# Kernel optimization log

Measured on AMD Instinct MI355X. Metric: run time of the kernel, lower is better.

## Reference

```python
import jax, jax.numpy as jnp
import numpy as np
from jax import lax

B, TS, NN, FC = 16, 16, 4096, 1
HIDDEN = 64


def setup_inputs() -> dict:
    key = jax.random.key(0)
    k1, k2, k3, k4, k5 = jax.random.split(key, 5)
    x = jax.random.normal(k1, (B, TS, NN, FC), dtype=jnp.float32)
    # Conv2d(in_ch + hidden -> 4*hidden, kernel=3, padding=1), OIHW layout
    conv_w = jax.random.normal(k2, (4 * HIDDEN, FC + HIDDEN, 3, 3), dtype=jnp.float32) * 0.05
    conv_b = jax.random.normal(k3, (4 * HIDDEN,), dtype=jnp.float32) * 0.05
    # fc: Conv2d(hidden -> 1, kernel=1)
    fc_w = jax.random.normal(k4, (1, HIDDEN, 1, 1), dtype=jnp.float32) * 0.05
    fc_b = jax.random.normal(k5, (1,), dtype=jnp.float32) * 0.05
    return {"x": x, "conv_w": conv_w, "conv_b": conv_b, "fc_w": fc_w, "fc_b": fc_b}


def _convlstm_forward(x, conv_w, conv_b, fc_w, fc_b):
    Bb, Ts, Nn, Fc = x.shape
    hidden = fc_w.shape[1]
    # [B, Ts, Fc, Nn, 1] -> scan over time axis: [Ts, B, Fc, Nn, 1]
    xp = jnp.transpose(x, (0, 1, 3, 2))[..., None]
    xs = jnp.swapaxes(xp, 0, 1)
    h0 = jnp.zeros((Bb, hidden, Nn, 1), dtype=x.dtype)
    c0 = jnp.zeros_like(h0)

    dn = lax.conv_dimension_numbers(h0.shape[:1] + (Fc + hidden, Nn, 1), conv_w.shape, ("NCHW", "OIHW", "NCHW"))

    def step(carry, xt):
        h, c = carry
        inp = jnp.concatenate([xt, h], axis=1)  # [B, Fc+hidden, Nn, 1]
        gates = lax.conv_general_dilated(inp, conv_w, (1, 1), ((1, 1), (1, 1)), dimension_numbers=dn)
        gates = gates + conv_b[None, :, None, None]
        i, f, o, g = jnp.split(gates, 4, axis=1)
        c2 = jax.nn.sigmoid(f) * c + jax.nn.sigmoid(i) * jnp.tanh(g)
        h2 = jax.nn.sigmoid(o) * jnp.tanh(c2)
        return (h2, c2), None

    (h, c), _ = lax.scan(step, (h0, c0), xs)
    # fc: 1x1 conv -> [B, 1, Nn, 1]
    out = jnp.einsum("bchw,oc->bohw", h, fc_w[:, :, 0, 0]) + fc_b[None, :, None, None]
    out = out[..., 0]                 # [B, 1, Nn]
    out = jnp.transpose(out, (0, 2, 1))[:, None]  # [B, 1, Nn, 1]
    return jnp.broadcast_to(out, (Bb, Ts, Nn, 1))


def reference(x, conv_w, conv_b, fc_w, fc_b):
    return _convlstm_forward(x, conv_w, conv_b, fc_w, fc_b)
```

## Files before the change

kernel.cpp:

```cpp
#include <hip/hip_runtime.h>

typedef _Float16 f16;
typedef __attribute__((ext_vector_type(8))) _Float16 half8;
typedef __attribute__((ext_vector_type(4))) float floatx4;

#define BB    16
#define TSN   16
#define NNP   4096
#define HID   64
#define KPK   224
#define WOUT  128
#define HALO  16
#define WCMP  160
#define HROWS 162
#define NMS   10
#define NTIL  32

#define LOG2E 1.44269504088896340736f

__device__ __forceinline__ int hadr(int rr, int c) {
    return rr * 64 + ((c ^ (rr & 7)) << 3);
}
__device__ __forceinline__ unsigned f16pair(float a, float b) {
    union { f16 h; unsigned short u; } ua, ub;
    ua.h = (f16)a; ub.h = (f16)b;
    return (unsigned)ua.u | ((unsigned)ub.u << 16);
}
__device__ __forceinline__ unsigned pkrtz(float a, float b) {
    typedef __fp16 h2v __attribute__((ext_vector_type(2)));
    h2v r = __builtin_amdgcn_cvt_pkrtz(a, b);
    union { h2v h; unsigned u; } cv; cv.h = r; return cv.u;
}

__device__ __forceinline__ float fast_exp2(float x) {
#if __has_builtin(__builtin_amdgcn_exp2f)
    return __builtin_amdgcn_exp2f(x);
#else
    return exp2f(x);
#endif
}
__device__ __forceinline__ float fast_rcp(float x) {
#if __has_builtin(__builtin_amdgcn_rcpf)
    return __builtin_amdgcn_rcpf(x);
#else
    return 1.0f / x;
#endif
}

__device__ __forceinline__ float dpp_xor8(float v) {
    return __int_as_float(__builtin_amdgcn_mov_dpp(__float_as_int(v), 0x128, 0xF, 0xF, true));
}
__device__ __forceinline__ float dpp_xor1(float v) {
    return __int_as_float(__builtin_amdgcn_mov_dpp(__float_as_int(v), 0xB1, 0xF, 0xF, true));
}

__global__ void pack_w_kernel(const float* __restrict__ conv_w,
                              const float* __restrict__ conv_b,
                              f16* __restrict__ wpack) {
    int idx = blockIdx.x * 256 + threadIdx.x;
    if (idx >= 4 * 64 * KPK) return;
    int k  = idx % KPK;
    int oc = idx / KPK;
    int kt = k >> 5, c = k & 31;
    float w = 0.0f;
    if (kt < 6) {
        int tap = kt >> 1;
        int j   = (kt & 1) * 32 + c;
        w = conv_w[((oc * 65 + 1 + j) * 3 + tap) * 3 + 1];
    } else if (c < 3) {
        w = conv_w[((oc * 65 + 0) * 3 + c) * 3 + 1];
    } else if (c == 3) {
        w = conv_b[oc];
    }
    float scale = (oc >= 192) ? (2.0f * LOG2E) : (-LOG2E);
    wpack[oc * KPK + k] = (f16)(w * scale);
}

template <int MS>
__device__ __forceinline__ void do_mfx(
    const f16* __restrict__ xts, const half8 (&bf)[7][2],
    const floatx4& zacc, floatx4 (&acc)[2], int m)
{
    const int ar = MS * 16 + m;
    half8 a = *(const half8*)(xts + ar * 8);
    acc[0] = __builtin_amdgcn_mfma_f32_16x16x32_f16(a, bf[6][0], zacc, 0, 0, 0);
    acc[1] = __builtin_amdgcn_mfma_f32_16x16x32_f16(a, bf[6][1], zacc, 0, 0, 0);
}

template <int MS>
__device__ __forceinline__ void do_mfh(
    const f16* __restrict__ hrd, const half8 (&bf)[7][2],
    floatx4 (&acc)[2], int m, int kg)
{
    const int ar = MS * 16 + m;
    __builtin_amdgcn_s_setprio(1);
#pragma unroll
    for (int kt = 0; kt < 6; ++kt) {
        half8 a = *(const half8*)(hrd + hadr(ar + (kt >> 1), (kt & 1) * 4 + kg));
        acc[0] = __builtin_amdgcn_mfma_f32_16x16x32_f16(a, bf[kt][0], acc[0], 0, 0, 0);
        acc[1] = __builtin_amdgcn_mfma_f32_16x16x32_f16(a, bf[kt][1], acc[1], 0, 0, 0);
    }
    __builtin_amdgcn_s_setprio(0);
}

template <int MS>
__device__ __forceinline__ void do_epi(
    f16* __restrict__ hwr, floatx4 (&acc)[2], float (&creg)[NMS * 2],
    int m, int kg, int wave, bool lowm, bool edge, int n0)
{
    float pg[2][2];
#pragma unroll
    for (int q = 0; q < 2; ++q)
#pragma unroll
        for (int j = 0; j < 2; ++j) {
            float send = lowm ? acc[q][2 + j] : acc[q][j];
            pg[q][j] = dpp_xor8(send);
        }

    float Y[2][4];
#pragma unroll
    for (int j = 0; j < 2; ++j) {
        Y[j][0] = lowm ? acc[0][j] : pg[0][j];
        Y[j][1] = lowm ? pg[0][j] : acc[0][2 + j];
        Y[j][2] = lowm ? acc[1][j] : pg[1][j];
        Y[j][3] = lowm ? pg[1][j] : acc[1][2 + j];
    }
    float E[2][4];
#pragma unroll
    for (int j = 0; j < 2; ++j)
#pragma unroll
        for (int g = 0; g < 4; ++g) E[j][g] = fast_exp2(Y[j][g]);

#pragma unroll
    for (int j = 0; j < 2; ++j) {
        int r  = lowm ? j : 2 + j;
        float Fi = 1.0f + E[j][0], Ff = 1.0f + E[j][1];
        float Fo = 1.0f + E[j][2], Fg = 1.0f + E[j][3];
        const int ridx = MS * 2 + j;
        float P  = Fi * Fg;
        float N  = fmaf(E[j][3] - 1.0f, Ff, creg[ridx] * P);
        float cn = N * fast_rcp(P * Ff);
        float Ec = fast_exp2(cn * (2.0f * LOG2E));
        float hnf = (Ec - 1.0f) * fast_rcp(Fo * (1.0f + Ec));
        creg[ridx] = cn;
        int rit = MS * 16 + kg * 4 + r;
        if (edge) {
            int pos = n0 - HALO + rit;
            if (pos < 0 || pos >= NNP) hnf = 0.0f;
        }
        float po = dpp_xor1(hnf);
        if (!(m & 1)) {
            int rr = rit + 1;
            ((unsigned*)hwr)[rr * 32 + ((wave ^ (rr & 7)) << 2) + ((m & 7) >> 1)] =
                pkrtz(hnf, po);
        }
    }
}

__global__ __launch_bounds__(512, 2)
void lstm_kernel(const float* __restrict__ x, const f16* __restrict__ wpack,
                 const float* __restrict__ fc_w, const float* __restrict__ fc_b,
                 float* __restrict__ out)
{
    __shared__ __align__(16) f16 hlds[2][HROWS * 64];
    __shared__ __align__(16) f16 xt[8 * WCMP * 8];

    const int blk  = blockIdx.x;
    const int b    = blk >> 5;
    const int tau  = blk & 31;
    const int n0   = tau * WOUT;
    const int tid  = threadIdx.x;
    const int lane = tid & 63;
    const int wave = tid >> 6;
    const int m    = lane & 15;
    const int kg   = lane >> 4;
    const int gh   = m >> 3;
    const int hid  = wave * 8 + (m & 7);
    const bool lowm = (m < 8);
    const bool edge = (tau == 0) || (tau == NTIL - 1);

    half8 bf[7][2];
#pragma unroll
    for (int kt = 0; kt < 7; ++kt)
#pragma unroll
        for (int q = 0; q < 2; ++q)
            bf[kt][q] = *(const half8*)(wpack + (size_t)((q * 2 + gh) * 64 + hid) * KPK + kt * 32 + kg * 8);

    const floatx4 zacc = {0.0f, 0.0f, 0.0f, 0.0f};

    float creg[NMS * 2];
#pragma unroll
    for (int i = 0; i < NMS * 2; ++i) creg[i] = 0.0f;

    auto stage_x = [&](int base) {
        for (int i = tid; i < 8 * WCMP; i += 512) {
            int ss = i / WCMP, r = i - ss * WCMP;
            const float* xb = x + ((size_t)b * TSN + base + ss) * NNP;
            int p = n0 - HALO + r;
            float v0 = (p - 1 >= 0 && p - 1 < NNP) ? xb[p - 1] : 0.0f;
            float v1 = (p >= 0 && p < NNP) ? xb[p] : 0.0f;
            float v2 = (p + 1 >= 0 && p + 1 < NNP) ? xb[p + 1] : 0.0f;
            unsigned* q = (unsigned*)(xt + (size_t)i * 8);
            q[0] = f16pair(v0, v1);
            q[1] = f16pair(v2, 1.0f);
            q[2] = 0u; q[3] = 0u;
        }
    };
    stage_x(0);

    for (int i = tid; i < HROWS * 64; i += 512) { hlds[0][i] = (f16)0; hlds[1][i] = (f16)0; }

#pragma unroll 1
    for (int s = 0; s < TSN; ++s) {
        if (s == 8) {
            __syncthreads();
            stage_x(8);
        }
        __syncthreads();

        const f16* hrd = hlds[s & 1];
        f16*       hwr = hlds[(s & 1) ^ 1];
        const f16* xts = xt + (size_t)(s & 7) * WCMP * 8;

        floatx4 accA[2], accB[2];
#define MFF(MS, A) do { do_mfx<MS>(xts, bf, zacc, A, m); do_mfh<MS>(hrd, bf, A, m, kg); } while (0)
#define EP(MS, A)  do_epi<MS>(hwr, A, creg, m, kg, wave, lowm, edge, n0)
        if (wave < 4) {
            MFF(0, accA);
            MFF(1, accB); EP(0, accA);
            MFF(2, accA); EP(1, accB);
            MFF(3, accB); EP(2, accA);
            MFF(4, accA); EP(3, accB);
            MFF(5, accB); EP(4, accA);
            MFF(6, accA); EP(5, accB);
            MFF(7, accB); EP(6, accA);
            MFF(8, accA); EP(7, accB);
            MFF(9, accB); EP(8, accA);
            EP(9, accB);
        } else {
            MFF(5, accA);
            MFF(6, accB); EP(5, accA);
            MFF(7, accA); EP(6, accB);
            MFF(8, accB); EP(7, accA);
            MFF(9, accA); EP(8, accB);
            MFF(0, accB); EP(9, accA);
            MFF(1, accA); EP(0, accB);
            MFF(2, accB); EP(1, accA);
            MFF(3, accA); EP(2, accB);
            MFF(4, accB); EP(3, accA);
            EP(4, accB);
        }
#undef MFF
#undef EP
    }
    __syncthreads();

    {
        const int part = tid & 3, row = tid >> 2;
        float fw[16];
#pragma unroll
        for (int e = 0; e < 16; ++e) fw[e] = fc_w[part * 16 + e];
        const int rr = row + HALO + 1;
        float ssum = 0.0f;
#pragma unroll
        for (int cc = 0; cc < 2; ++cc) {
            half8 v = *(const half8*)(hlds[0] + hadr(rr, part * 2 + cc));
#pragma unroll
            for (int e = 0; e < 8; ++e) ssum += (float)v[e] * fw[cc * 8 + e];
        }
        ssum += __shfl_xor(ssum, 1);
        ssum += __shfl_xor(ssum, 2);
        float* srow = (float*)xt;
        if (part == 0) srow[row] = ssum + fc_b[0];
        __syncthreads();
        for (int i = tid; i < WOUT * TSN; i += 512) {
            int tt = i >> 7, r2 = i & (WOUT - 1);
            out[((size_t)b * TSN + tt) * NNP + n0 + r2] = srow[r2];
        }
    }
}

extern "C" void kernel_launch(void* const* d_in, const int* in_sizes, int n_in,
                              void* d_out, int out_size, void* d_ws, size_t ws_size,
                              hipStream_t stream) {
    const float* x      = (const float*)d_in[0];
    const float* conv_w = (const float*)d_in[1];
    const float* conv_b = (const float*)d_in[2];
    const float* fc_w   = (const float*)d_in[3];
    const float* fc_b   = (const float*)d_in[4];
    float* out = (float*)d_out;

    f16* wpack = (f16*)d_ws;

    pack_w_kernel<<<(4 * 64 * KPK + 255) / 256, 256, 0, stream>>>(conv_w, conv_b, wpack);
    lstm_kernel<<<BB * NTIL, 512, 0, stream>>>(x, wpack, fc_w, fc_b, out);
}
```

Baseline: 249.8 us.

## Prepack x im2col into global workspace and read directly, overlapping x MFMAs with barrier

Adds a separate kernel that packs x into the f16 3-tap im2col layout in global memory, once per batch and timestep. The LSTM kernel then reads these A-fragments straight from global/L2 instead of staging them in LDS. This removes the x staging loop, the extra barriers at step 8, and the x LDS buffer. The x-projection MFMAs for the first two sub-tiles are issued before the per-step barrier so they overlap with it. In exchange it adds a kernel launch and global-memory traffic, and global-load latency now sits inside the recurrent loop.

```diff
diff --git a/kernel.cpp b/kernel.cpp
--- a/kernel.cpp
+++ b/kernel.cpp
@@ -3,6 +3,7 @@
 typedef _Float16 f16;
 typedef __attribute__((ext_vector_type(8))) _Float16 half8;
 typedef __attribute__((ext_vector_type(4))) float floatx4;
+typedef __attribute__((ext_vector_type(4))) unsigned uint4v;
 
 #define BB    16
 #define TSN   16
@@ -15,6 +16,7 @@
 #define HROWS 162
 #define NMS   10
 #define NTIL  32
+#define XROWS (NNP + 2 * HALO)
 
 #define LOG2E 1.44269504088896340736f
 
@@ -76,13 +78,27 @@
     wpack[oc * KPK + k] = (f16)(w * scale);
 }
 
+__global__ void pack_x_kernel(const float* __restrict__ x, f16* __restrict__ xpack) {
+    int idx = blockIdx.x * 256 + threadIdx.x;
+    if (idx >= BB * TSN * XROWS) return;
+    int pp = idx % XROWS;
+    int bs = idx / XROWS;
+    int p  = pp - HALO;
+    const float* xb = x + (size_t)bs * NNP;
+    float v0 = (p - 1 >= 0 && p - 1 < NNP) ? xb[p - 1] : 0.0f;
+    float v1 = (p >= 0 && p < NNP) ? xb[p] : 0.0f;
+    float v2 = (p + 1 >= 0 && p + 1 < NNP) ? xb[p + 1] : 0.0f;
+    uint4v q = { f16pair(v0, v1), f16pair(v2, 1.0f), 0u, 0u };
+    *(uint4v*)(xpack + (size_t)idx * 8) = q;
+}
+
 template <int MS>
 __device__ __forceinline__ void do_mfx(
-    const f16* __restrict__ xts, const half8 (&bf)[7][2],
+    const f16* __restrict__ xs, const half8 (&bf)[7][2],
     const floatx4& zacc, floatx4 (&acc)[2], int m)
 {
     const int ar = MS * 16 + m;
-    half8 a = *(const half8*)(xts + ar * 8);
+    half8 a = *(const half8*)(xs + (size_t)ar * 8);
     acc[0] = __builtin_amdgcn_mfma_f32_16x16x32_f16(a, bf[6][0], zacc, 0, 0, 0);
     acc[1] = __builtin_amdgcn_mfma_f32_16x16x32_f16(a, bf[6][1], zacc, 0, 0, 0);
 }
@@ -158,12 +174,11 @@
 }
 
 __global__ __launch_bounds__(512, 2)
-void lstm_kernel(const float* __restrict__ x, const f16* __restrict__ wpack,
+void lstm_kernel(const f16* __restrict__ xpack, const f16* __restrict__ wpack,
                  const float* __restrict__ fc_w, const float* __restrict__ fc_b,
                  float* __restrict__ out)
 {
     __shared__ __align__(16) f16 hlds[2][HROWS * 64];
-    __shared__ __align__(16) f16 xt[8 * WCMP * 8];
 
     const int blk  = blockIdx.x;
     const int b    = blk >> 5;
@@ -192,42 +207,29 @@
 #pragma unroll
     for (int i = 0; i < NMS * 2; ++i) creg[i] = 0.0f;
 
-    auto stage_x = [&](int base) {
-        for (int i = tid; i < 8 * WCMP; i += 512) {
-            int ss = i / WCMP, r = i - ss * WCMP;
-            const float* xb = x + ((size_t)b * TSN + base + ss) * NNP;
-            int p = n0 - HALO + r;
-            float v0 = (p - 1 >= 0 && p - 1 < NNP) ? xb[p - 1] : 0.0f;
-            float v1 = (p >= 0 && p < NNP) ? xb[p] : 0.0f;
-            float v2 = (p + 1 >= 0 && p + 1 < NNP) ? xb[p + 1] : 0.0f;
-            unsigned* q = (unsigned*)(xt + (size_t)i * 8);
-            q[0] = f16pair(v0, v1);
-            q[1] = f16pair(v2, 1.0f);
-            q[2] = 0u; q[3] = 0u;
-        }
-    };
-    stage_x(0);
-
     for (int i = tid; i < HROWS * 64; i += 512) { hlds[0][i] = (f16)0; hlds[1][i] = (f16)0; }
+
+    const f16* xp0 = xpack + ((size_t)b * TSN * XROWS + n0) * 8;
 
 #pragma unroll 1
     for (int s = 0; s < TSN; ++s) {
-        if (s == 8) {
-            __syncthreads();
-            stage_x(8);
-        }
-        __syncthreads();
-
         const f16* hrd = hlds[s & 1];
         f16*       hwr = hlds[(s & 1) ^ 1];
-        const f16* xts = xt + (size_t)(s & 7) * WCMP * 8;
+        const f16* xs  = xp0 + (size_t)s * XROWS * 8;
 
         floatx4 accA[2], accB[2];
-#define MFF(MS, A) do { do_mfx<MS>(xts, bf, zacc, A, m); do_mfh<MS>(hrd, bf, A, m, kg); } while (0)
+#define MFX(MS, A) do_mfx<MS>(xs, bf, zacc, A, m)
+#define MFH(MS, A) do_mfh<MS>(hrd, bf, A, m, kg)
+#define MFF(MS, A) do { MFX(MS, A); MFH(MS, A); } while (0)
 #define EP(MS, A)  do_epi<MS>(hwr, A, creg, m, kg, wave, lowm, edge, n0)
+        if (wave < 4) { MFX(0, accA); MFX(1, accB); }
+        else          { MFX(5, accA); MFX(6, accB); }
+
+        __syncthreads();
+
         if (wave < 4) {
-            MFF(0, accA);
-            MFF(1, accB); EP(0, accA);
+            MFH(0, accA);
+            MFH(1, accB); EP(0, accA);
             MFF(2, accA); EP(1, accB);
             MFF(3, accB); EP(2, accA);
             MFF(4, accA); EP(3, accB);
@@ -238,8 +240,8 @@
             MFF(9, accB); EP(8, accA);
             EP(9, accB);
         } else {
-            MFF(5, accA);
-            MFF(6, accB); EP(5, accA);
+            MFH(5, accA);
+            MFH(6, accB); EP(5, accA);
             MFF(7, accA); EP(6, accB);
             MFF(8, accB); EP(7, accA);
             MFF(9, accA); EP(8, accB);
@@ -250,6 +252,8 @@
             MFF(4, accB); EP(3, accA);
             EP(4, accB);
         }
+#undef MFX
+#undef MFH
 #undef MFF
 #undef EP
     }
@@ -270,7 +274,7 @@
         }
         ssum += __shfl_xor(ssum, 1);
         ssum += __shfl_xor(ssum, 2);
-        float* srow = (float*)xt;
+        float* srow = (float*)hlds[1];
         if (part == 0) srow[row] = ssum + fc_b[0];
         __syncthreads();
         for (int i = tid; i < WOUT * TSN; i += 512) {
@@ -290,8 +294,11 @@
     const float* fc_b   = (const float*)d_in[4];
     float* out = (float*)d_out;
 
-    f16* wpack = (f16*)d_ws;
+    char* ws = (char*)d_ws;
+    f16* wpack = (f16*)ws;
+    f16* xpack = (f16*)(ws + 131072);
 
     pack_w_kernel<<<(4 * 64 * KPK + 255) / 256, 256, 0, stream>>>(conv_w, conv_b, wpack);
-    lstm_kernel<<<BB * NTIL, 512, 0, stream>>>(x, wpack, fc_w, fc_b, out);
-}
+    pack_x_kernel<<<(BB * TSN * XROWS + 255) / 256, 256, 0, stream>>>(x, xpack);
+    lstm_kernel<<<BB * NTIL, 512, 0, stream>>>(xpack, wpack, fc_w, fc_b, out);
+}
```

Result: slower. 278.1 us (+11.3%).

## Peel first and last timesteps to skip zero-h MFMAs and unneeded halo rows

Applied to the files above, without the earlier changes.

Peels timestep 0 so it runs only the input-term MFMAs, because h is zero and the hidden-state MFMAs are skipped. Peels the final timestep so it computes only the inner row tiles that feed the output, dropping the outermost halo tiles. Zero-initialisation of the LDS h buffers is reduced to the boundary rows, and the s_setprio wrapping around the hidden MFMA loop is removed. The trimmed tile lists and partial initialisation depend on halo-validity reasoning, so any wrong boundary assumption would corrupt edge results.

```diff
diff --git a/kernel.cpp b/kernel.cpp
--- a/kernel.cpp
+++ b/kernel.cpp
@@ -93,14 +93,12 @@
     floatx4 (&acc)[2], int m, int kg)
 {
     const int ar = MS * 16 + m;
-    __builtin_amdgcn_s_setprio(1);
 #pragma unroll
     for (int kt = 0; kt < 6; ++kt) {
         half8 a = *(const half8*)(hrd + hadr(ar + (kt >> 1), (kt & 1) * 4 + kg));
         acc[0] = __builtin_amdgcn_mfma_f32_16x16x32_f16(a, bf[kt][0], acc[0], 0, 0, 0);
         acc[1] = __builtin_amdgcn_mfma_f32_16x16x32_f16(a, bf[kt][1], acc[1], 0, 0, 0);
     }
-    __builtin_amdgcn_s_setprio(0);
 }
 
 template <int MS>
@@ -208,10 +206,36 @@
     };
     stage_x(0);
 
-    for (int i = tid; i < HROWS * 64; i += 512) { hlds[0][i] = (f16)0; hlds[1][i] = (f16)0; }
+    for (int i = tid; i < 4 * 64; i += 512) {
+        int buf = i >> 7, rr = ((i >> 6) & 1) ? (HROWS - 1) : 0;
+        hlds[buf][rr * 64 + (i & 63)] = (f16)0;
+    }
+
+    __syncthreads();
+
+    {
+        f16* hwr = hlds[1];
+        const f16* xts = xt;
+        floatx4 accA[2], accB[2];
+#define MFX(MS, A) do_mfx<MS>(xts, bf, zacc, A, m)
+#define EP(MS, A)  do_epi<MS>(hwr, A, creg, m, kg, wave, lowm, edge, n0)
+        MFX(0, accA);
+        MFX(1, accB); EP(0, accA);
+        MFX(2, accA); EP(1, accB);
+        MFX(3, accB); EP(2, accA);
+        MFX(4, accA); EP(3, accB);
+        MFX(5, accB); EP(4, accA);
+        MFX(6, accA); EP(5, accB);
+        MFX(7, accB); EP(6, accA);
+        MFX(8, accA); EP(7, accB);
+        MFX(9, accB); EP(8, accA);
+        EP(9, accB);
+#undef MFX
+#undef EP
+    }
 
 #pragma unroll 1
-    for (int s = 0; s < TSN; ++s) {
+    for (int s = 1; s < TSN - 1; ++s) {
         if (s == 8) {
             __syncthreads();
             stage_x(8);
@@ -253,6 +277,40 @@
 #undef MFF
 #undef EP
     }
+
+    {
+        __syncthreads();
+        const f16* hrd = hlds[1];
+        f16*       hwr = hlds[0];
+        const f16* xts = xt + (size_t)7 * WCMP * 8;
+
+        floatx4 accA[2], accB[2];
+#define MFF(MS, A) do { do_mfx<MS>(xts, bf, zacc, A, m); do_mfh<MS>(hrd, bf, A, m, kg); } while (0)
+#define EP(MS, A)  do_epi<MS>(hwr, A, creg, m, kg, wave, lowm, edge, n0)
+        if (wave < 4) {
+            MFF(1, accA);
+            MFF(2, accB); EP(1, accA);
+            MFF(3, accA); EP(2, accB);
+            MFF(4, accB); EP(3, accA);
+            MFF(5, accA); EP(4, accB);
+            MFF(6, accB); EP(5, accA);
+            MFF(7, accA); EP(6, accB);
+            MFF(8, accB); EP(7, accA);
+            EP(8, accB);
+        } else {
+            MFF(5, accA);
+            MFF(6, accB); EP(5, accA);
+            MFF(7, accA); EP(6, accB);
+            MFF(8, accB); EP(7, accA);
+            MFF(1, accA); EP(8, accB);
+            MFF(2, accB); EP(1, accA);
+            MFF(3, accA); EP(2, accB);
+            MFF(4, accB); EP(3, accA);
+            EP(4, accB);
+        }
+#undef MFF
+#undef EP
+    }
     __syncthreads();
 
     {
```

New measurement: 234.4 us. 1.07x faster.
